# Kernel optimization log

Hardware: AMD Instinct MI355X
Metric: run time of the kernel (lower is better)

Reference implementation:

```python
import jax, jax.numpy as jnp
from jax import lax
import numpy as np

N_LAYERS = 2
HIDDEN = 1024
N_STOCKS = 1024
LB, UB = 0.0, 0.2
REBAL_ITERS = 32  # fixed upper bound; loop converges in 1-2 iters in practice


def setup_inputs() -> dict:
    key = jax.random.key(0)
    ks = jax.random.split(key, 20)
    B, T = 512, 128
    inp = {"x": jax.random.normal(ks[0], (B, T, N_STOCKS), dtype=jnp.float32)}
    k = 1
    for l in range(N_LAYERS):
        in_dim = N_STOCKS if l == 0 else HIDDEN
        s = 1.0 / np.sqrt(HIDDEN)
        inp[f"w_ih_{l}"] = jax.random.uniform(ks[k], (3 * HIDDEN, in_dim), minval=-s, maxval=s); k += 1
        inp[f"w_hh_{l}"] = jax.random.uniform(ks[k], (3 * HIDDEN, HIDDEN), minval=-s, maxval=s); k += 1
        inp[f"b_ih_{l}"] = jax.random.uniform(ks[k], (3 * HIDDEN,), minval=-s, maxval=s); k += 1
        inp[f"b_hh_{l}"] = jax.random.uniform(ks[k], (3 * HIDDEN,), minval=-s, maxval=s); k += 1
    s = 1.0 / np.sqrt(HIDDEN)
    inp["fc_w"] = jax.random.uniform(ks[k], (N_STOCKS, HIDDEN), minval=-s, maxval=s); k += 1
    inp["fc_b"] = jax.random.uniform(ks[k], (N_STOCKS,), minval=-s, maxval=s)
    return inp


def _gru_layer(x, w_ih, w_hh, b_ih, b_hh):
    # x: [B,T,D] -> hidden sequence [B,T,H]; PyTorch GRU cell math
    B, T, _ = x.shape
    H = w_hh.shape[1]
    x_proj = jnp.einsum('btd,gd->btg', x, w_ih) + b_ih  # [B,T,3H]

    def step(h, xp):
        hp = h @ w_hh.T + b_hh
        xr, xz, xn = jnp.split(xp, 3, axis=-1)
        hr, hz, hn = jnp.split(hp, 3, axis=-1)
        r = jax.nn.sigmoid(xr + hr)
        z = jax.nn.sigmoid(xz + hz)
        n = jnp.tanh(xn + r * hn)
        h_new = (1.0 - z) * n + z * h
        return h_new, h_new

    h0 = jnp.zeros((B, H), x.dtype)
    _, hs = lax.scan(step, h0, jnp.swapaxes(x_proj, 0, 1))  # [T,B,H]
    return jnp.swapaxes(hs, 0, 1)


def _rebalance(w, lb, ub, n_iters=REBAL_ITERS):
    # Batched version of the iterative capped-simplex redistribution loop.
    old = w
    wc = jnp.clip(w, lb, ub)
    done = jnp.zeros((w.shape[0],), dtype=bool)

    def body(state, _):
        old, wc, done = state
        leftover = jnp.sum(old - wc, axis=-1, keepdims=True)            # [B,1]
        mask = wc != ub                                                  # nominees
        num = jnp.sum(mask, axis=-1)                                     # [B]
        nom_sum = jnp.sum(jnp.where(mask, wc, 0.0), axis=-1, keepdims=True)
        gift = leftover * wc / jnp.where(nom_sum == 0.0, 1.0, nom_sum)
        wc_new = jnp.where(mask, wc + gift, wc)
        no_nom = num == 0
        over = jnp.any(wc_new > ub, axis=-1)
        new_done = done | no_nom | (~over)
        wc_next = jnp.where(no_nom[:, None], wc,
                            jnp.where(over[:, None], jnp.clip(wc_new, lb, ub), wc_new))
        old_next = jnp.where(no_nom[:, None], old, wc_new)
        wc_out = jnp.where(done[:, None], wc, wc_next)
        old_out = jnp.where(done[:, None], old, old_next)
        return (old_out, wc_out, new_done), None

    (_, wc, _), _ = lax.scan(body, (old, wc, done), None, length=n_iters)
    return wc


def reference(x, w_ih_0, w_hh_0, b_ih_0, b_hh_0, w_ih_1, w_hh_1, b_ih_1, b_hh_1, fc_w, fc_b):
    h = _gru_layer(x, w_ih_0, w_hh_0, b_ih_0, b_hh_0)
    h = _gru_layer(h, w_ih_1, w_hh_1, b_ih_1, b_hh_1)
    h_t = h[:, -1, :]                                   # last time step [B,H]
    logit = h_t @ fc_w.T + fc_b                         # dropout is identity in eval
    logit = jax.nn.silu(logit)
    probs = jax.nn.softmax(logit, axis=-1)
    return _rebalance(probs, LB, UB)
```

## Files before the change

### kernel.cpp

```cpp
#include <hip/hip_runtime.h>
#include <hip/hip_bf16.h>
#include <stdint.h>

#define BB 512
#define TT 128
#define DD 1024
#define HH 1024
#define G3 3072
#define TC 32
#define NCH (TT/TC)
#define NRING 33

typedef __bf16 bft;
typedef __bf16 bf16x8 __attribute__((ext_vector_type(8)));
typedef float f32x4 __attribute__((ext_vector_type(4)));

__device__ __forceinline__ void gl_lds16(const bft* g, void* lds_base_uniform) {
  __builtin_amdgcn_global_load_lds(
      (const __attribute__((address_space(1))) void*)g,
      (__attribute__((address_space(3))) void*)lds_base_uniform,
      16, 0, 0);
}

__device__ __forceinline__ void st_wt_bf16(bft* p, float v) {
  bft h = (bft)v;
  union { bft h; unsigned short u; } cv; cv.h = h;
  unsigned int uv = cv.u;
  asm volatile("global_store_short %0, %1, off sc0 sc1" :: "v"(p), "v"(uv) : "memory");
}
__device__ __forceinline__ void st_wt_f32(float* p, float v) {
  asm volatile("global_store_dword %0, %1, off sc0 sc1" :: "v"(p), "v"(v) : "memory");
}
__device__ __forceinline__ void st_wt_u32(int* p, int v) {
  asm volatile("global_store_dword %0, %1, off sc0 sc1" :: "v"(p), "v"(v) : "memory");
}
__device__ __forceinline__ int ld_co_u32(const int* p) {
  int v;
  asm volatile("global_load_dword %0, %1, off sc0 sc1\n\ts_waitcnt vmcnt(0)"
               : "=v"(v) : "v"(p) : "memory");
  return v;
}

__device__ __forceinline__ float fexp2(float x) {
  float r; asm("v_exp_f32 %0, %1" : "=v"(r) : "v"(x)); return r;
}
__device__ __forceinline__ float frcp(float x) {
  float r; asm("v_rcp_f32 %0, %1" : "=v"(r) : "v"(x)); return r;
}
#define LOG2E 1.44269504f

__global__ void k_cvt(const float* __restrict__ in, bft* __restrict__ out, long n) {
  long i = ((long)blockIdx.x * blockDim.x + threadIdx.x) * 8;
  long stride = (long)gridDim.x * blockDim.x * 8;
  for (; i < n; i += stride) {
    float4 a = *(const float4*)(in + i);
    float4 b = *(const float4*)(in + i + 4);
    bf16x8 r;
    r[0] = (bft)a.x; r[1] = (bft)a.y; r[2] = (bft)a.z; r[3] = (bft)a.w;
    r[4] = (bft)b.x; r[5] = (bft)b.y; r[6] = (bft)b.z; r[7] = (bft)b.w;
    *(bf16x8*)(out + i) = r;
  }
}

template<int AMODE, int EPI>
__launch_bounds__(256)
__global__ void k_gemm(const void* __restrict__ Ap, long lda,
                       const bft* __restrict__ W, long ldw,
                       const float* __restrict__ bias,
                       void* __restrict__ Cout, long ldc,
                       int t0, int K) {
  __shared__ unsigned char sm[32768];
  const int tid  = threadIdx.x;
  const int lane = tid & 63;
  const int wid  = tid >> 6;
  const int m0 = blockIdx.y * 128;
  const int n0 = blockIdx.x * 128;
  const int wm = wid >> 1, wn = wid & 1;

  f32x4 acc[4][4] = {};

  for (int k0 = 0; k0 < K; k0 += 64) {
    if (AMODE == 1) {
      const float* Af = (const float*)Ap;
#pragma unroll
      for (int s = 0; s < 4; ++s) {
        int seg = wid * 4 + s;
        int row = seg * 8 + (lane >> 3);
        int mr = m0 + row;
        long grow = (long)(mr >> 5) * TT + t0 + (mr & 31);
        const float* src = Af + grow * lda + k0 + (lane & 7) * 8;
        float4 a  = *(const float4*)src;
        float4 b2 = *(const float4*)(src + 4);
        bf16x8 r;
        r[0] = (bft)a.x;  r[1] = (bft)a.y;  r[2] = (bft)a.z;  r[3] = (bft)a.w;
        r[4] = (bft)b2.x; r[5] = (bft)b2.y; r[6] = (bft)b2.z; r[7] = (bft)b2.w;
        *(bf16x8*)(sm + seg * 1024 + (lane >> 3) * 128 +
                   (((lane & 7) * 16) ^ ((row & 7) << 4))) = r;
      }
    } else {
      const bft* Ab = (const bft*)Ap;
#pragma unroll
      for (int s = 0; s < 4; ++s) {
        int seg = wid * 4 + s;
        int row = seg * 8 + (lane >> 3);
        int cbs = ((lane & 7) * 16) ^ ((row & 7) << 4);
        int mr = m0 + row;
        long grow;
        if (AMODE == 0) grow = mr;
        else { int sl = t0 + (mr & 31); if (sl >= NRING) sl -= NRING;
               grow = (long)sl * BB + (mr >> 5); }
        gl_lds16(Ab + grow * lda + k0 + (cbs >> 1), sm + seg * 1024);
      }
    }
#pragma unroll
    for (int s = 0; s < 4; ++s) {
      int seg = wid * 4 + s;
      int row = seg * 8 + (lane >> 3);
      int cbs = ((lane & 7) * 16) ^ ((row & 7) << 4);
      gl_lds16(W + (long)(n0 + row) * ldw + k0 + (cbs >> 1), sm + 16384 + seg * 1024);
    }
    __syncthreads();
#pragma unroll
    for (int ks = 0; ks < 2; ++ks) {
      int kb = ks * 64 + (lane >> 4) * 16;
      bf16x8 aF[4], bF[4];
#pragma unroll
      for (int mi = 0; mi < 4; ++mi) {
        int row = wm * 64 + mi * 16 + (lane & 15);
        aF[mi] = *(const bf16x8*)(sm + row * 128 + (kb ^ ((row & 7) << 4)));
      }
#pragma unroll
      for (int ni = 0; ni < 4; ++ni) {
        int row = wn * 64 + ni * 16 + (lane & 15);
        bF[ni] = *(const bf16x8*)(sm + 16384 + row * 128 + (kb ^ ((row & 7) << 4)));
      }
#pragma unroll
      for (int mi = 0; mi < 4; ++mi)
#pragma unroll
        for (int ni = 0; ni < 4; ++ni)
          acc[mi][ni] = __builtin_amdgcn_mfma_f32_16x16x32_bf16(aF[mi], bF[ni], acc[mi][ni], 0, 0, 0);
    }
    __syncthreads();
  }

#pragma unroll
  for (int mi = 0; mi < 4; ++mi)
#pragma unroll
    for (int ni = 0; ni < 4; ++ni) {
      int col = n0 + wn * 64 + ni * 16 + (lane & 15);
      float bv = bias[col];
#pragma unroll
      for (int r = 0; r < 4; ++r) {
        long row = m0 + wm * 64 + mi * 16 + (lane >> 4) * 4 + r;
        float v = acc[mi][ni][r] + bv;
        if (EPI == 0) {
          ((bft*)Cout)[row * ldc + col] = (bft)v;
        } else {
          ((float*)Cout)[row * ldc + col] = v / (1.f + expf(-v));
        }
      }
    }
}

__launch_bounds__(256, 1)
__global__ void k_persist(const bft* __restrict__ whh, const float* __restrict__ bhh,
                          const bft* __restrict__ xp,
                          bft* __restrict__ ring,
                          float* __restrict__ hfc, int* __restrict__ flags,
                          int t0s, int first, int pbase) {
  __shared__ unsigned char sm[98304];
  unsigned char* smW = sm;
  unsigned char* smA = sm + 32768;

  const int tid  = threadIdx.x;
  const int lane = tid & 63;
  const int wid  = tid >> 6;
  const int bid  = blockIdx.x;
  const int xcd = bid & 7, loc = bid >> 3;
  const int mt = xcd >> 1;
  const int nt = (xcd & 1) * 32 + loc;
  const int j0 = nt * 16;
  const int m0 = mt * 128;
  const int j  = j0 + (lane & 15);
  int* gflags = flags + mt * 64;

#pragma unroll
  for (int s8 = 0; s8 < 8; ++s8) {
    int s = wid * 8 + s8;
    int row = s >> 1;
    int half = s & 1;
    int hb = half * 1024 + lane * 16;
    int sb = hb ^ ((row & 7) << 4);
    long grow = (long)(2 * 1024 + j0 + row);
    gl_lds16(whh + grow * 1024 + (sb >> 1), smW + s * 1024);
  }

  bf16x8 wrz[2][16][2];
#pragma unroll
  for (int g = 0; g < 2; ++g) {
    const bft* wbase = whh + (((long)g * 1024 + j) << 10) + ((lane >> 4) * 8);
#pragma unroll
    for (int k = 0; k < 16; ++k)
#pragma unroll
      for (int ks = 0; ks < 2; ++ks) {
        bf16x8 wl = *(const bf16x8*)(wbase + k * 64 + ks * 32);
        asm("" : "=a"(wrz[g][k][ks]) : "0"(wl));
      }
  }
  asm volatile("s_waitcnt vmcnt(0)" ::: "memory");
  __builtin_amdgcn_s_barrier();

  const float br = bhh[j], bz = bhh[1024 + j], bn = bhh[2048 + j];

  auto stageA = [&](const bft* base, int k0, int bufsel) {
    unsigned char* dst = smA + bufsel * 16384;
#pragma unroll
    for (int si = 0; si < 4; ++si) {
      int seg = wid * 4 + si;
      int row = seg * 8 + (lane >> 3);
      int cb = ((lane & 7) * 16) ^ ((row & 7) << 4);
      gl_lds16(base + (long)(m0 + row) * DD + k0 + (cb >> 1), dst + seg * 1024);
    }
  };

  float xg[3][2][4];
  float hp[2][4];

  auto prefXG = [&](int s) {
#pragma unroll
    for (int mi = 0; mi < 2; ++mi)
#pragma unroll
      for (int r = 0; r < 4; ++r) {
        long b = m0 + wid * 32 + mi * 16 + (lane >> 4) * 4 + r;
        long xrow = (b * TC + s) * (long)G3 + j;
        xg[0][mi][r] = (float)xp[xrow];
        xg[1][mi][r] = (float)xp[xrow + 1024];
        xg[2][mi][r] = (float)xp[xrow + 2048];
      }
  };

  prefXG(0);
  if (first) {
#pragma unroll
    for (int mi = 0; mi < 2; ++mi)
#pragma unroll
      for (int r = 0; r < 4; ++r) hp[mi][r] = 0.f;
  } else {
#pragma unroll
    for (int mi = 0; mi < 2; ++mi)
#pragma unroll
      for (int r = 0; r < 4; ++r) {
        long b = m0 + wid * 32 + mi * 16 + (lane >> 4) * 4 + r;
        hp[mi][r] = hfc[b * HH + j];
      }
  }
  __builtin_amdgcn_sched_barrier(0);

  for (int s = 0; s < TC; ++s) {
    if (s) {
      int target = pbase + s;
      if (tid < 64) {
        const int* fp = gflags + tid;
        while (ld_co_u32(fp) < target) __builtin_amdgcn_s_sleep(2);
      }
      __syncthreads();
    }

    int sl = t0s + s; if (sl >= NRING) sl -= NRING;
    int psl = sl ? sl - 1 : NRING - 1;

    f32x4 acc[3][2] = {};
    if (!(first && s == 0)) {
      const bft* Ab = ring + (long)psl * (BB * (long)DD);
      stageA(Ab, 0, 0);
      stageA(Ab, 64, 1);
      stageA(Ab, 128, 2);
#pragma unroll
      for (int k = 0; k < 16; ++k) {
        __builtin_amdgcn_s_barrier();
        if (k < 13) stageA(Ab, (k + 3) * 64, (k + 3) & 3);
        if (k < 13)       asm volatile("s_waitcnt vmcnt(12)" ::: "memory");
        else if (k == 13) asm volatile("s_waitcnt vmcnt(8)" ::: "memory");
        else if (k == 14) asm volatile("s_waitcnt vmcnt(4)" ::: "memory");
        else              asm volatile("s_waitcnt vmcnt(0)" ::: "memory");
        __builtin_amdgcn_s_barrier();
        __builtin_amdgcn_sched_barrier(0);
        const unsigned char* Abuf = smA + (k & 3) * 16384;
#pragma unroll
        for (int ks = 0; ks < 2; ++ks) {
          int kb = ks * 64 + (lane >> 4) * 16;
          bf16x8 aF[2];
#pragma unroll
          for (int mi = 0; mi < 2; ++mi) {
            int row = wid * 32 + mi * 16 + (lane & 15);
            aF[mi] = *(const bf16x8*)(Abuf + row * 128 + (kb ^ ((row & 7) << 4)));
          }
          int wrow = lane & 15;
          bf16x8 bFn = *(const bf16x8*)(smW + wrow * 2048 +
                                        ((k * 128 + kb) ^ ((wrow & 7) << 4)));
#pragma unroll
          for (int mi = 0; mi < 2; ++mi) {
            acc[0][mi] = __builtin_amdgcn_mfma_f32_16x16x32_bf16(aF[mi], wrz[0][k][ks], acc[0][mi], 0, 0, 0);
            acc[1][mi] = __builtin_amdgcn_mfma_f32_16x16x32_bf16(aF[mi], wrz[1][k][ks], acc[1][mi], 0, 0, 0);
            acc[2][mi] = __builtin_amdgcn_mfma_f32_16x16x32_bf16(aF[mi], bFn,           acc[2][mi], 0, 0, 0);
          }
        }
      }
    }

    bft* outp = ring + (long)sl * (BB * (long)DD);
#pragma unroll
    for (int mi = 0; mi < 2; ++mi)
#pragma unroll
      for (int r = 0; r < 4; ++r) {
        long b = m0 + wid * 32 + mi * 16 + (lane >> 4) * 4 + r;
        float hr = acc[0][mi][r] + br;
        float hz = acc[1][mi][r] + bz;
        float hn = acc[2][mi][r] + bn;
        float rg = frcp(1.f + fexp2(-LOG2E * (xg[0][mi][r] + hr)));
        float zg = frcp(1.f + fexp2(-LOG2E * (xg[1][mi][r] + hz)));
        float e2 = fexp2(2.f * LOG2E * (xg[2][mi][r] + rg * hn));
        float ng = 1.f - 2.f * frcp(e2 + 1.f);
        float hv = (1.f - zg) * ng + zg * hp[mi][r];
        hp[mi][r] = hv;
        st_wt_bf16(outp + b * DD + j, hv);
        if (s == TC - 1) st_wt_f32(hfc + b * HH + j, hv);
      }

    __syncthreads();
    if (s < TC - 1) {
      if (tid == 0) st_wt_u32(gflags + nt, pbase + s + 1);
      prefXG(s + 1);
      __builtin_amdgcn_sched_barrier(0);
    }
  }
}

__device__ __forceinline__ float blk_sum(float v, float* red, int tid) {
#pragma unroll
  for (int o = 32; o; o >>= 1) v += __shfl_xor(v, o);
  if ((tid & 63) == 0) red[tid >> 6] = v;
  __syncthreads();
  v = red[0] + red[1] + red[2] + red[3];
  __syncthreads();
  return v;
}
__device__ __forceinline__ float blk_max(float v, float* red, int tid) {
#pragma unroll
  for (int o = 32; o; o >>= 1) v = fmaxf(v, __shfl_xor(v, o));
  if ((tid & 63) == 0) red[tid >> 6] = v;
  __syncthreads();
  v = fmaxf(fmaxf(red[0], red[1]), fmaxf(red[2], red[3]));
  __syncthreads();
  return v;
}

__launch_bounds__(256)
__global__ void k_smrebal(const float* __restrict__ logits, float* __restrict__ out) {
  __shared__ float red[4];
  const int tid = threadIdx.x;
  const long row = blockIdx.x;
  const float ub = 0.2f, lb = 0.0f;
  float4 lv = *(const float4*)(logits + row * 1024 + tid * 4);

  float m = fmaxf(fmaxf(lv.x, lv.y), fmaxf(lv.z, lv.w));
  m = blk_max(m, red, tid);
  float e[4] = {expf(lv.x - m), expf(lv.y - m), expf(lv.z - m), expf(lv.w - m)};
  float S = blk_sum(e[0] + e[1] + e[2] + e[3], red, tid);

  float old_[4], wc[4];
#pragma unroll
  for (int k = 0; k < 4; ++k) {
    float p = e[k] / S;
    old_[k] = p;
    wc[k] = fminf(fmaxf(p, lb), ub);
  }
  bool done = false;
  for (int it = 0; it < 32 && !done; ++it) {
    float d3 = 0.f, cnt = 0.f, nsum = 0.f;
#pragma unroll
    for (int k = 0; k < 4; ++k) {
      d3 += old_[k] - wc[k];
      bool mk = (wc[k] != ub);
      cnt += mk ? 1.f : 0.f;
      nsum += mk ? wc[k] : 0.f;
    }
    float leftover = blk_sum(d3, red, tid);
    float num = blk_sum(cnt, red, tid);
    float nom_sum = blk_sum(nsum, red, tid);
    float denom = (nom_sum == 0.f) ? 1.f : nom_sum;
    float wcn[4], mx = -1e30f;
#pragma unroll
    for (int k = 0; k < 4; ++k) {
      bool mk = (wc[k] != ub);
      wcn[k] = mk ? wc[k] + leftover * wc[k] / denom : wc[k];
      mx = fmaxf(mx, wcn[k]);
    }
    float gmx = blk_max(mx, red, tid);
    bool no_nom = (num == 0.f);
    bool over = (gmx > ub);
#pragma unroll
    for (int k = 0; k < 4; ++k) {
      float nxt = no_nom ? wc[k] : (over ? fminf(fmaxf(wcn[k], lb), ub) : wcn[k]);
      float oldn = no_nom ? old_[k] : wcn[k];
      wc[k] = nxt;
      old_[k] = oldn;
    }
    done = no_nom || !over;
  }
#pragma unroll
  for (int k = 0; k < 4; ++k) out[row * 1024 + tid * 4 + k] = wc[k];
}

extern "C" void kernel_launch(void* const* d_in, const int* in_sizes, int n_in,
                              void* d_out, int out_size, void* d_ws, size_t ws_size,
                              hipStream_t stream) {
  const float* x      = (const float*)d_in[0];
  const float* wih[2] = {(const float*)d_in[1], (const float*)d_in[5]};
  const float* whh[2] = {(const float*)d_in[2], (const float*)d_in[6]};
  const float* bih[2] = {(const float*)d_in[3], (const float*)d_in[7]};
  const float* bhh[2] = {(const float*)d_in[4], (const float*)d_in[8]};
  const float* fcw    = (const float*)d_in[9];
  const float* fcb    = (const float*)d_in[10];
  float* outp = (float*)d_out;

  unsigned char* ws = (unsigned char*)d_ws;
  size_t off = 0;
  auto alloc = [&](size_t bytes) -> void* {
    void* p = ws + off;
    off += (bytes + 255) & ~(size_t)255;
    return p;
  };
  bft* wihb0   = (bft*)alloc((size_t)G3 * DD * 2);
  bft* whhb0   = (bft*)alloc((size_t)G3 * HH * 2);
  bft* wihb1   = (bft*)alloc((size_t)G3 * HH * 2);
  bft* whhb1   = (bft*)alloc((size_t)G3 * HH * 2);
  bft* fcwb    = (bft*)alloc((size_t)1024 * 1024 * 2);
  bft* xp      = (bft*)alloc((size_t)BB * TC * G3 * 2);
  bft* ring0   = (bft*)alloc((size_t)NRING * BB * DD * 2);
  bft* ring1   = (bft*)alloc((size_t)NRING * BB * DD * 2);
  float* hfc0  = (float*)alloc((size_t)BB * HH * 4);
  float* hfc1  = (float*)alloc((size_t)BB * HH * 4);
  int* flags   = (int*)alloc(1024);
  float* logits= (float*)alloc((size_t)BB * 1024 * 4);
  if (off > ws_size) return;

  hipMemsetAsync(flags, 0, 1024, stream);

  k_cvt<<<dim3(1536), dim3(256), 0, stream>>>(wih[0], wihb0, (long)G3 * DD);
  k_cvt<<<dim3(1536), dim3(256), 0, stream>>>(whh[0], whhb0, (long)G3 * HH);
  k_cvt<<<dim3(1536), dim3(256), 0, stream>>>(wih[1], wihb1, (long)G3 * HH);
  k_cvt<<<dim3(1536), dim3(256), 0, stream>>>(whh[1], whhb1, (long)G3 * HH);
  k_cvt<<<dim3(512),  dim3(256), 0, stream>>>(fcw, fcwb, (long)1024 * 1024);

  for (int c = 0; c < NCH; ++c) {
    int t0 = c * TC;
    int t0s = t0 % NRING;
    int first = (c == 0) ? 1 : 0;
    k_gemm<1, 0><<<dim3(G3 / 128, (BB * TC) / 128), 256, 0, stream>>>(
        x, DD, wihb0, DD, bih[0], xp, G3, t0, DD);
    k_persist<<<dim3(256), dim3(256), 0, stream>>>(
        whhb0, bhh[0], xp, ring0, hfc0, flags, t0s, first, (2 * c) * TC);
    k_gemm<2, 0><<<dim3(G3 / 128, (BB * TC) / 128), 256, 0, stream>>>(
        ring0, DD, wihb1, DD, bih[1], xp, G3, t0s, DD);
    k_persist<<<dim3(256), dim3(256), 0, stream>>>(
        whhb1, bhh[1], xp, ring1, hfc1, flags, t0s, first, (2 * c + 1) * TC);
  }
  const bft* hfin = ring1 + (size_t)((TT - 1) % NRING) * BB * DD;
  k_gemm<0, 1><<<dim3(1024 / 128, BB / 128), 256, 0, stream>>>(
      hfin, DD, fcwb, HH, fcb, logits, 1024, 0, HH);
  k_smrebal<<<dim3(BB), 256, 0, stream>>>(logits, outp);
}
```

Baseline: 2.677 ms.

## Load recurrent A operand directly into registers instead of staging through LDS

The per-step hidden-state tile was previously staged from the ring buffer into a 4-deep LDS ring with global_load_lds, guarded by barriers and explicit vmcnt waits. Each wave now issues direct global vector loads of its own MFMA A fragments into a 4-slot register pipeline, prefetching three k-steps ahead. This removes the LDS traffic and the two block barriers per k iteration, and shrinks shared memory. The cost is more VGPR pressure, uncoalesced 16-byte row-strided global loads, and reliance on compiler-inserted waits instead of explicit ones.

New measurement: 5.273 ms. 97.0% more time.

```diff
diff --git a/kernel.cpp b/kernel.cpp
--- a/kernel.cpp
+++ b/kernel.cpp
@@ -168,9 +168,8 @@
                           bft* __restrict__ ring,
                           float* __restrict__ hfc, int* __restrict__ flags,
                           int t0s, int first, int pbase) {
-  __shared__ unsigned char sm[98304];
+  __shared__ unsigned char sm[32768];
   unsigned char* smW = sm;
-  unsigned char* smA = sm + 32768;
 
   const int tid  = threadIdx.x;
   const int lane = tid & 63;
@@ -212,17 +211,6 @@
 
   const float br = bhh[j], bz = bhh[1024 + j], bn = bhh[2048 + j];
 
-  auto stageA = [&](const bft* base, int k0, int bufsel) {
-    unsigned char* dst = smA + bufsel * 16384;
-#pragma unroll
-    for (int si = 0; si < 4; ++si) {
-      int seg = wid * 4 + si;
-      int row = seg * 8 + (lane >> 3);
-      int cb = ((lane & 7) * 16) ^ ((row & 7) << 4);
-      gl_lds16(base + (long)(m0 + row) * DD + k0 + (cb >> 1), dst + seg * 1024);
-    }
-  };
-
   float xg[3][2][4];
   float hp[2][4];
 
@@ -271,38 +259,44 @@
 
     f32x4 acc[3][2] = {};
     if (!(first && s == 0)) {
-      const bft* Ab = ring + (long)psl * (BB * (long)DD);
-      stageA(Ab, 0, 0);
-      stageA(Ab, 64, 1);
-      stageA(Ab, 128, 2);
+      const bft* Abase = ring + (long)psl * (BB * (long)DD);
+      const bft* aptr[2][2];
+#pragma unroll
+      for (int mi = 0; mi < 2; ++mi)
+#pragma unroll
+        for (int ks = 0; ks < 2; ++ks)
+          aptr[mi][ks] = Abase + (long)(m0 + wid * 32 + mi * 16 + (lane & 15)) * DD
+                         + ks * 32 + (lane >> 4) * 8;
+
+      bf16x8 pipe[4][2][2];
+#pragma unroll
+      for (int kp = 0; kp < 3; ++kp)
+#pragma unroll
+        for (int mi = 0; mi < 2; ++mi)
+#pragma unroll
+          for (int ks = 0; ks < 2; ++ks)
+            pipe[kp][mi][ks] = *(const bf16x8*)(aptr[mi][ks] + kp * 64);
+
 #pragma unroll
       for (int k = 0; k < 16; ++k) {
-        __builtin_amdgcn_s_barrier();
-        if (k < 13) stageA(Ab, (k + 3) * 64, (k + 3) & 3);
-        if (k < 13)       asm volatile("s_waitcnt vmcnt(12)" ::: "memory");
-        else if (k == 13) asm volatile("s_waitcnt vmcnt(8)" ::: "memory");
-        else if (k == 14) asm volatile("s_waitcnt vmcnt(4)" ::: "memory");
-        else              asm volatile("s_waitcnt vmcnt(0)" ::: "memory");
-        __builtin_amdgcn_s_barrier();
-        __builtin_amdgcn_sched_barrier(0);
-        const unsigned char* Abuf = smA + (k & 3) * 16384;
+        if (k < 13) {
+#pragma unroll
+          for (int mi = 0; mi < 2; ++mi)
+#pragma unroll
+            for (int ks = 0; ks < 2; ++ks)
+              pipe[(k + 3) & 3][mi][ks] = *(const bf16x8*)(aptr[mi][ks] + (k + 3) * 64);
+        }
 #pragma unroll
         for (int ks = 0; ks < 2; ++ks) {
           int kb = ks * 64 + (lane >> 4) * 16;
-          bf16x8 aF[2];
-#pragma unroll
-          for (int mi = 0; mi < 2; ++mi) {
-            int row = wid * 32 + mi * 16 + (lane & 15);
-            aF[mi] = *(const bf16x8*)(Abuf + row * 128 + (kb ^ ((row & 7) << 4)));
-          }
           int wrow = lane & 15;
           bf16x8 bFn = *(const bf16x8*)(smW + wrow * 2048 +
                                         ((k * 128 + kb) ^ ((wrow & 7) << 4)));
 #pragma unroll
           for (int mi = 0; mi < 2; ++mi) {
-            acc[0][mi] = __builtin_amdgcn_mfma_f32_16x16x32_bf16(aF[mi], wrz[0][k][ks], acc[0][mi], 0, 0, 0);
-            acc[1][mi] = __builtin_amdgcn_mfma_f32_16x16x32_bf16(aF[mi], wrz[1][k][ks], acc[1][mi], 0, 0, 0);
-            acc[2][mi] = __builtin_amdgcn_mfma_f32_16x16x32_bf16(aF[mi], bFn,           acc[2][mi], 0, 0, 0);
+            acc[0][mi] = __builtin_amdgcn_mfma_f32_16x16x32_bf16(pipe[k & 3][mi][ks], wrz[0][k][ks], acc[0][mi], 0, 0, 0);
+            acc[1][mi] = __builtin_amdgcn_mfma_f32_16x16x32_bf16(pipe[k & 3][mi][ks], wrz[1][k][ks], acc[1][mi], 0, 0, 0);
+            acc[2][mi] = __builtin_amdgcn_mfma_f32_16x16x32_bf16(pipe[k & 3][mi][ks], bFn,           acc[2][mi], 0, 0, 0);
           }
         }
       }
```
